# Performance work log

Measured on AMD Instinct MI355X. Metric: run time of the kernel, lower is better.

The kernel has to match this reference:

```python
import jax, jax.numpy as jnp
import numpy as np

D_MODEL = 512
N_HEADS = 16
D_HEAD = D_MODEL // N_HEADS


def _relative_shift(pos_score):
    # pos_score: [B, H, T, T]  (Transformer-XL shift trick)
    B, H, T1, T2 = pos_score.shape
    padded = jnp.pad(pos_score, ((0, 0), (0, 0), (0, 0), (1, 0)))  # [B,H,T1,T2+1]
    padded = padded.reshape(B, H, T2 + 1, T1)
    return padded[:, :, 1:].reshape(B, H, T1, T2)


def setup_inputs() -> dict:
    key = jax.random.key(0)
    ks = jax.random.split(key, 12)
    B, T, D = 4, 1024, D_MODEL
    s = 1.0 / np.sqrt(D)
    return {
        "q": jax.random.normal(ks[0], (B, T, D), jnp.float32),
        "k": jax.random.normal(ks[1], (B, T, D), jnp.float32),
        "v": jax.random.normal(ks[2], (B, T, D), jnp.float32),
        "pos_embedding": jax.random.normal(ks[3], (B, T, D), jnp.float32),
        "Wq": jax.random.normal(ks[4], (D, D), jnp.float32) * s,
        "bq": jnp.zeros((D,), jnp.float32),
        "Wp": jax.random.normal(ks[5], (D, D), jnp.float32) * s,
        "Wf": jax.random.normal(ks[6], (D, D), jnp.float32) * s,
        "bf": jnp.zeros((D,), jnp.float32),
        "u_bias": jax.random.normal(ks[7], (N_HEADS, D_HEAD), jnp.float32) * s,
        "v_bias": jax.random.normal(ks[8], (N_HEADS, D_HEAD), jnp.float32) * s,
    }


def reference(q, k, v, pos_embedding, Wq, bq, Wp, Wf, bf, u_bias, v_bias):
    B, T, D = q.shape
    H, Dh = N_HEADS, D_HEAD
    sqrt_dim = jnp.asarray(np.sqrt(D_MODEL), q.dtype)
    # NOTE: original module uses linear_q for q, k AND v (faithful to source)
    qh = (q @ Wq + bq).reshape(B, T, H, Dh)            # [B,T,H,Dh]
    kh = (k @ Wq + bq).reshape(B, T, H, Dh)
    vh = (v @ Wq + bq).reshape(B, T, H, Dh)
    ph = (pos_embedding @ Wp).reshape(B, T, H, Dh)     # no bias

    content_score = jnp.einsum('bthd,bshd->bhts', qh + u_bias, kh)
    pos_score = jnp.einsum('bthd,bshd->bhts', qh + v_bias, ph)
    pos_score = _relative_shift(pos_score)

    score = (content_score + pos_score) / sqrt_dim     # [B,H,T,T]
    attn = jax.nn.softmax(score, axis=-1)              # dropout identity in eval
    context = jnp.einsum('bhts,bshd->bthd', attn, vh).reshape(B, T, D)
    return context @ Wf + bf
```

## Files before the change

### kernel.cpp

```cpp
#include <hip/hip_runtime.h>
#include <hip/hip_bf16.h>

typedef __bf16 bf16;
typedef bf16 bf16x8 __attribute__((ext_vector_type(8)));
typedef bf16 bf16x4 __attribute__((ext_vector_type(4)));
typedef float f32x4 __attribute__((ext_vector_type(4)));

#define SCALE_INV_SQRT_D 0.04419417382415922f


__global__ __launch_bounds__(256) void prep_kernel(
    const float* __restrict__ Wq, const float* __restrict__ Wp, const float* __restrict__ Wf,
    bf16* __restrict__ WqT, bf16* __restrict__ WpT, bf16* __restrict__ WfT,
    bf16* __restrict__ phx)
{
  const int tid = threadIdx.x;
  if (blockIdx.x < 192) {
    __shared__ bf16 t[64][72];
    const int m = blockIdx.x >> 6;
    const int tb = blockIdx.x & 63;
    const int tr = tb >> 3, tc = tb & 7;
    const float* W = (m == 0) ? Wq : (m == 1) ? Wp : Wf;
    bf16*        O = (m == 0) ? WqT : (m == 1) ? WpT : WfT;
    const int r = tid >> 2, cg = tid & 3;
    {
      const float* src = W + (size_t)(tr * 64 + r) * 512 + tc * 64 + cg * 16;
      f32x4 a = *(const f32x4*)src, b2 = *(const f32x4*)(src + 4);
      f32x4 c = *(const f32x4*)(src + 8), d = *(const f32x4*)(src + 12);
      bf16x8 lo, hi;
#pragma unroll
      for (int j = 0; j < 4; j++) { lo[j] = (bf16)a[j]; lo[4 + j] = (bf16)b2[j]; hi[j] = (bf16)c[j]; hi[4 + j] = (bf16)d[j]; }
      *(bf16x8*)(&t[r][cg * 16])     = lo;
      *(bf16x8*)(&t[r][cg * 16 + 8]) = hi;
    }
    __syncthreads();
    bf16x8 o0, o1;
#pragma unroll
    for (int j = 0; j < 8; j++) { o0[j] = t[cg * 16 + j][r]; o1[j] = t[cg * 16 + 8 + j][r]; }
    bf16* dst = O + (size_t)(tc * 64 + r) * 512 + tr * 64 + cg * 16;
    *(bf16x8*)dst = o0;
    *(bf16x8*)(dst + 8) = o1;
  } else {
    int z = (blockIdx.x - 192) * 256 + tid;
    int bh = z >> 6;
    int rsel = (z >> 5) & 1;
    int d = z & 31;
    phx[((size_t)bh * 2048 + (rsel ? 2047 : 1024)) * 32 + d] = (bf16)0.0f;
  }
}

__global__ __launch_bounds__(256) void proj_gemm(
    const float* __restrict__ q, const float* __restrict__ k, const float* __restrict__ v,
    const float* __restrict__ pos,
    const bf16* __restrict__ WqT, const bf16* __restrict__ WpT, const float* __restrict__ bq,
    bf16* __restrict__ qh, bf16* __restrict__ kh, bf16* __restrict__ vT, bf16* __restrict__ phx)
{
  __shared__ float Asf[128 * 36];
  __shared__ bf16  Bs[128 * 40];
  const int tid = threadIdx.x;
  const int wave = tid >> 6, lane = tid & 63, quad = lane >> 4, ln = lane & 15;
  const int tn = blockIdx.x & 3;
  const int tm = blockIdx.x >> 2;
  const int kind = tm >> 5;
  const int rr0 = (tm & 31) * 128;
  const float* X = (kind == 0) ? q : (kind == 1) ? k : (kind == 2) ? v : pos;
  const bf16* WT = ((kind < 3) ? WqT : WpT) + (size_t)tn * 128 * 512;
  const int qm = (wave & 1) * 64, qn = (wave >> 1) * 64;
  const int srow = tid >> 2, scg = tid & 3;

  f32x4 acc[4][4] = {};

  for (int kk = 0; kk < 16; kk++) {
    const int k0 = kk * 32;
    {
      const float* p0 = X + (size_t)(rr0 + srow) * 512 + k0 + scg * 8;
      const float* p1 = X + (size_t)(rr0 + srow + 64) * 512 + k0 + scg * 8;
      *(f32x4*)(Asf + srow * 36 + scg * 8)            = *(const f32x4*)p0;
      *(f32x4*)(Asf + srow * 36 + scg * 8 + 4)        = *(const f32x4*)(p0 + 4);
      *(f32x4*)(Asf + (srow + 64) * 36 + scg * 8)     = *(const f32x4*)p1;
      *(f32x4*)(Asf + (srow + 64) * 36 + scg * 8 + 4) = *(const f32x4*)(p1 + 4);
    }
    *(bf16x8*)(Bs + srow * 40 + scg * 8)        = *(const bf16x8*)(WT + (size_t)srow * 512 + k0 + scg * 8);
    *(bf16x8*)(Bs + (srow + 64) * 40 + scg * 8) = *(const bf16x8*)(WT + (size_t)(srow + 64) * 512 + k0 + scg * 8);
    __syncthreads();
    bf16x8 af[4], bfm[4];
#pragma unroll
    for (int i = 0; i < 4; i++) {
      f32x4 lo = *(const f32x4*)(Asf + (qm + i * 16 + ln) * 36 + quad * 8);
      f32x4 hi = *(const f32x4*)(Asf + (qm + i * 16 + ln) * 36 + quad * 8 + 4);
      bf16x8 t;
#pragma unroll
      for (int j = 0; j < 4; j++) { t[j] = (bf16)lo[j]; t[4 + j] = (bf16)hi[j]; }
      af[i] = t;
      bfm[i] = *(const bf16x8*)(Bs + (qn + i * 16 + ln) * 40 + quad * 8);
    }
#pragma unroll
    for (int i = 0; i < 4; i++)
#pragma unroll
      for (int j = 0; j < 4; j++)
        acc[i][j] = __builtin_amdgcn_mfma_f32_16x16x32_bf16(af[i], bfm[j], acc[i][j], 0, 0, 0);
    __syncthreads();
  }

#pragma unroll
  for (int i = 0; i < 4; i++)
#pragma unroll
    for (int j = 0; j < 4; j++) {
      const int nn = tn * 128 + qn + j * 16 + ln;
      const int hh = nn >> 5, dd = nn & 31;
      const float bias = (kind < 3) ? bq[nn] : 0.0f;
#pragma unroll
      for (int r = 0; r < 4; r++) {
        const int rr = rr0 + qm + i * 16 + quad * 4 + r;
        const int bb = rr >> 10, tt = rr & 1023;
        const bf16 o = (bf16)(acc[i][j][r] + bias);
        const size_t base = (size_t)(bb * 16 + hh);
        if (kind == 0)      qh[(base * 1024 + tt) * 32 + dd] = o;
        else if (kind == 1) kh[(base * 1024 + tt) * 32 + dd] = o;
        else if (kind == 2) vT[(base * 32 + dd) * 1024 + tt] = o;
        else {
          phx[(base * 2048 + tt) * 32 + dd] = o;
          if (tt <= 1021) phx[(base * 2048 + tt + 1025) * 32 + dd] = o;
        }
      }
    }
}

__global__ __launch_bounds__(256, 4) void attn_kernel(
    const bf16* __restrict__ qh, const bf16* __restrict__ kh,
    const bf16* __restrict__ vT, const bf16* __restrict__ phx,
    const float* __restrict__ u_bias, const float* __restrict__ v_bias,
    bf16* __restrict__ ctx)
{
  __shared__ float fs[4 * 16 * 84];
  __shared__ bf16  pb[4 * 16 * 72];

  const int tid = threadIdx.x;
  const int wave = tid >> 6, lane = tid & 63, quad = lane >> 4, ln = lane & 15;
  const int wg = blockIdx.x;
  const int bh = wg & 63, tq = wg >> 6;
  const int h = bh & 15, b = bh >> 4;
  const int t0 = tq * 64;
  const bf16* qh_h  = qh  + (size_t)bh * 1024 * 32;
  const bf16* kh_h  = kh  + (size_t)bh * 1024 * 32;
  const bf16* vT_h  = vT  + (size_t)bh * 32 * 1024;
  const bf16* phx_h = phx + (size_t)bh * 2048 * 32;

  float* fsw = fs + wave * 16 * 84;
  bf16*  pbw = pb + wave * 16 * 72;

  bf16x8 qu, qva, qvn;
  {
    const int t = t0 + wave * 16 + ln;
    bf16x8 q0 = *(const bf16x8*)(qh_h + (size_t)t * 32 + quad * 8);
    bf16x8 q1 = *(const bf16x8*)(qh_h + (size_t)(t + 1) * 32 + quad * 8);
    const float* ubp = u_bias + h * 32 + quad * 8;
    const float* vbp = v_bias + h * 32 + quad * 8;
#pragma unroll
    for (int j = 0; j < 8; j++) {
      qu[j]  = (bf16)((float)q0[j] + ubp[j]);
      qva[j] = (bf16)((float)q0[j] + vbp[j]);
      qvn[j] = (bf16)((float)q1[j] + vbp[j]);
    }
  }

  f32x4 O0 = {0.f, 0.f, 0.f, 0.f}, O1 = {0.f, 0.f, 0.f, 0.f};
  float m_run = -1e30f, l_run = 0.0f;
  const f32x4 zf = {0.f, 0.f, 0.f, 0.f};

  for (int si = 0; si < 16; si++) {
    const int s0 = si * 64;
    const int j0 = s0 - t0 + 960;
    const int jb0 = j0 + (3 - wave) * 16;

#pragma unroll
    for (int i = 0; i < 5; i++) {
      const int jrow = jb0 + i * 16 + ln;
      bf16x8 pbf = *(const bf16x8*)(phx_h + (size_t)jrow * 32 + quad * 8);
      bf16x8 bsel = (jb0 + i * 16 >= 1024) ? qvn : qva;
      f32x4 f = __builtin_amdgcn_mfma_f32_16x16x32_bf16(pbf, bsel, zf, 0, 0, 0);
      *(f32x4*)(fsw + ln * 84 + i * 16 + quad * 4) = f;
    }

    f32x4 c[4];
#pragma unroll
    for (int cs = 0; cs < 4; cs++) {
      bf16x8 kbf = *(const bf16x8*)(kh_h + (size_t)(s0 + cs * 16 + ln) * 32 + quad * 8);
      c[cs] = __builtin_amdgcn_mfma_f32_16x16x32_bf16(kbf, qu, zf, 0, 0, 0);
    }

    float sc_[4][4];
#pragma unroll
    for (int cs = 0; cs < 4; cs++)
#pragma unroll
      for (int r = 0; r < 4; r++) {
        const int col = cs * 16 + quad * 4 + r - ln + 15;
        sc_[cs][r] = (c[cs][r] + fsw[ln * 84 + col]) * SCALE_INV_SQRT_D;
      }

    float mt = sc_[0][0];
#pragma unroll
    for (int cs = 0; cs < 4; cs++)
#pragma unroll
      for (int r = 0; r < 4; r++) mt = fmaxf(mt, sc_[cs][r]);
    mt = fmaxf(mt, __shfl_xor(mt, 16));
    mt = fmaxf(mt, __shfl_xor(mt, 32));

    const float mnew = fmaxf(m_run, mt);
    const float al = __expf(m_run - mnew);
    float psum = 0.0f;
#pragma unroll
    for (int cs = 0; cs < 4; cs++) {
      bf16x4 pk;
#pragma unroll
      for (int r = 0; r < 4; r++) {
        const float p = __expf(sc_[cs][r] - mnew);
        psum += p;
        pk[r] = (bf16)p;
      }
      *(bf16x4*)(pbw + ln * 72 + cs * 16 + quad * 4) = pk;
    }
    psum += __shfl_xor(psum, 16);
    psum += __shfl_xor(psum, 32);
    l_run = l_run * al + psum;
    m_run = mnew;

#pragma unroll
    for (int r = 0; r < 4; r++) {
      const float alr = __shfl(al, ((lane >> 4) << 2) + r);
      O0[r] *= alr;
      O1[r] *= alr;
    }

#pragma unroll
    for (int kb = 0; kb < 2; kb++) {
      bf16x8 a  = *(const bf16x8*)(pbw + ln * 72 + kb * 32 + quad * 8);
      bf16x8 b0 = *(const bf16x8*)(vT_h + (size_t)ln * 1024 + s0 + kb * 32 + quad * 8);
      bf16x8 b1 = *(const bf16x8*)(vT_h + (size_t)(16 + ln) * 1024 + s0 + kb * 32 + quad * 8);
      O0 = __builtin_amdgcn_mfma_f32_16x16x32_bf16(a, b0, O0, 0, 0, 0);
      O1 = __builtin_amdgcn_mfma_f32_16x16x32_bf16(a, b1, O1, 0, 0, 0);
    }
  }

#pragma unroll
  for (int r = 0; r < 4; r++) {
    const float lr = __shfl(l_run, ((lane >> 4) << 2) + r);
    const float inv = 1.0f / lr;
    const int t = t0 + wave * 16 + quad * 4 + r;
    const size_t o = ((size_t)(b * 1024 + t)) * 512 + h * 32;
    ctx[o + ln]      = (bf16)(O0[r] * inv);
    ctx[o + 16 + ln] = (bf16)(O1[r] * inv);
  }
}

__global__ __launch_bounds__(256) void out_gemm(
    const bf16* __restrict__ ctx, const bf16* __restrict__ WfT, const float* __restrict__ bfv,
    float* __restrict__ out)
{
  __shared__ bf16 As[64 * 40];
  __shared__ bf16 Bs[128 * 40];
  const int tid = threadIdx.x;
  const int wave = tid >> 6, lane = tid & 63, quad = lane >> 4, ln = lane & 15;
  const int tn = blockIdx.x & 3;
  const int tm = blockIdx.x >> 2;
  const int rr0 = tm * 64;
  const bf16* WT = WfT + (size_t)tn * 128 * 512;
  const int qm = (wave & 1) * 32, qn = (wave >> 1) * 64;
  const int srow = tid >> 2, scg = tid & 3;

  f32x4 acc[2][4] = {};
  for (int kk = 0; kk < 16; kk++) {
    const int k0 = kk * 32;
    *(bf16x8*)(As + srow * 40 + scg * 8)        = *(const bf16x8*)(ctx + (size_t)(rr0 + srow) * 512 + k0 + scg * 8);
    *(bf16x8*)(Bs + srow * 40 + scg * 8)        = *(const bf16x8*)(WT + (size_t)srow * 512 + k0 + scg * 8);
    *(bf16x8*)(Bs + (srow + 64) * 40 + scg * 8) = *(const bf16x8*)(WT + (size_t)(srow + 64) * 512 + k0 + scg * 8);
    __syncthreads();
    bf16x8 af[2], bfm[4];
#pragma unroll
    for (int i = 0; i < 2; i++)
      af[i] = *(const bf16x8*)(As + (qm + i * 16 + ln) * 40 + quad * 8);
#pragma unroll
    for (int j = 0; j < 4; j++)
      bfm[j] = *(const bf16x8*)(Bs + (qn + j * 16 + ln) * 40 + quad * 8);
#pragma unroll
    for (int i = 0; i < 2; i++)
#pragma unroll
      for (int j = 0; j < 4; j++)
        acc[i][j] = __builtin_amdgcn_mfma_f32_16x16x32_bf16(af[i], bfm[j], acc[i][j], 0, 0, 0);
    __syncthreads();
  }

#pragma unroll
  for (int i = 0; i < 2; i++)
#pragma unroll
    for (int j = 0; j < 4; j++) {
      const int nn = tn * 128 + qn + j * 16 + ln;
      const float bias = bfv[nn];
#pragma unroll
      for (int r = 0; r < 4; r++) {
        const int rr = rr0 + qm + i * 16 + quad * 4 + r;
        out[(size_t)rr * 512 + nn] = acc[i][j][r] + bias;
      }
    }
}

extern "C" void kernel_launch(void* const* d_in, const int* in_sizes, int n_in,
                              void* d_out, int out_size, void* d_ws, size_t ws_size,
                              hipStream_t stream) {
  const float* q   = (const float*)d_in[0];
  const float* k   = (const float*)d_in[1];
  const float* v   = (const float*)d_in[2];
  const float* pe  = (const float*)d_in[3];
  const float* Wq  = (const float*)d_in[4];
  const float* bq  = (const float*)d_in[5];
  const float* Wp  = (const float*)d_in[6];
  const float* Wf  = (const float*)d_in[7];
  const float* bfv = (const float*)d_in[8];
  const float* ub  = (const float*)d_in[9];
  const float* vb  = (const float*)d_in[10];

  bf16* ws  = (bf16*)d_ws;
  bf16* qh  = ws;
  bf16* kh  = qh + 2097152;
  bf16* vT  = kh + 2097152;
  bf16* phx = vT + 2097152;
  bf16* ctx = phx + 4194304;
  bf16* WqT = ctx + 2097152;
  bf16* WpT = WqT + 262144;
  bf16* WfT = WpT + 262144;

  prep_kernel<<<208, 256, 0, stream>>>(Wq, Wp, Wf, WqT, WpT, WfT, phx);
  proj_gemm<<<512, 256, 0, stream>>>(q, k, v, pe, WqT, WpT, bq, qh, kh, vT, phx);
  attn_kernel<<<1024, 256, 0, stream>>>(qh, kh, vT, phx, ub, vb, ctx);
  out_gemm<<<256, 256, 0, stream>>>(ctx, WfT, bfv, (float*)d_out);
}
```

Baseline: 195.2 us.

## Fold softmax scale into query, use exp2, vectorize projection epilogue stores

The 1/sqrt(d)·log2(e) factor is folded into the biased query vectors, so the per-score multiply disappears and the softmax uses exp2f instead of __expf. The projection GEMM swaps the MFMA operand roles so each lane holds four consecutive output features, which lets the epilogue write bf16x4 vector stores and load bias as a float4 instead of scalar stores. The P staging buffer row stride is padded from 72 to 88 to change the LDS bank pattern. Rounding the scaled query to bf16 shifts numerics slightly, and the transposed vT stores stay scalar.

```diff
diff --git a/kernel.cpp b/kernel.cpp
--- a/kernel.cpp
+++ b/kernel.cpp
@@ -6,7 +6,7 @@
 typedef bf16 bf16x4 __attribute__((ext_vector_type(4)));
 typedef float f32x4 __attribute__((ext_vector_type(4)));
 
-#define SCALE_INV_SQRT_D 0.04419417382415922f
+#define SCALE_LOG2 0.06376237f
 
 
 __global__ __launch_bounds__(256) void prep_kernel(
@@ -65,7 +65,8 @@
   const int rr0 = (tm & 31) * 128;
   const float* X = (kind == 0) ? q : (kind == 1) ? k : (kind == 2) ? v : pos;
   const bf16* WT = ((kind < 3) ? WqT : WpT) + (size_t)tn * 128 * 512;
-  const int qm = (wave & 1) * 64, qn = (wave >> 1) * 64;
+  const int qn_ = (wave & 1) * 64;
+  const int qr_ = (wave >> 1) * 64;
   const int srow = tid >> 2, scg = tid & 3;
 
   f32x4 acc[4][4] = {};
@@ -83,47 +84,50 @@
     *(bf16x8*)(Bs + srow * 40 + scg * 8)        = *(const bf16x8*)(WT + (size_t)srow * 512 + k0 + scg * 8);
     *(bf16x8*)(Bs + (srow + 64) * 40 + scg * 8) = *(const bf16x8*)(WT + (size_t)(srow + 64) * 512 + k0 + scg * 8);
     __syncthreads();
-    bf16x8 af[4], bfm[4];
+    bf16x8 wf[4], xf[4];
 #pragma unroll
     for (int i = 0; i < 4; i++) {
-      f32x4 lo = *(const f32x4*)(Asf + (qm + i * 16 + ln) * 36 + quad * 8);
-      f32x4 hi = *(const f32x4*)(Asf + (qm + i * 16 + ln) * 36 + quad * 8 + 4);
+      wf[i] = *(const bf16x8*)(Bs + (qn_ + i * 16 + ln) * 40 + quad * 8);
+      f32x4 lo = *(const f32x4*)(Asf + (qr_ + i * 16 + ln) * 36 + quad * 8);
+      f32x4 hi = *(const f32x4*)(Asf + (qr_ + i * 16 + ln) * 36 + quad * 8 + 4);
       bf16x8 t;
 #pragma unroll
       for (int j = 0; j < 4; j++) { t[j] = (bf16)lo[j]; t[4 + j] = (bf16)hi[j]; }
-      af[i] = t;
-      bfm[i] = *(const bf16x8*)(Bs + (qn + i * 16 + ln) * 40 + quad * 8);
+      xf[i] = t;
     }
 #pragma unroll
     for (int i = 0; i < 4; i++)
 #pragma unroll
       for (int j = 0; j < 4; j++)
-        acc[i][j] = __builtin_amdgcn_mfma_f32_16x16x32_bf16(af[i], bfm[j], acc[i][j], 0, 0, 0);
-    __syncthreads();
-  }
-
-#pragma unroll
-  for (int i = 0; i < 4; i++)
+        acc[i][j] = __builtin_amdgcn_mfma_f32_16x16x32_bf16(wf[i], xf[j], acc[i][j], 0, 0, 0);
+    __syncthreads();
+  }
+
+#pragma unroll
+  for (int i = 0; i < 4; i++) {
+    const int nn0 = tn * 128 + qn_ + i * 16 + quad * 4;
+    const int dd0 = nn0 & 31, hh = nn0 >> 5;
+    f32x4 b4 = {0.f, 0.f, 0.f, 0.f};
+    if (kind < 3) b4 = *(const f32x4*)(bq + nn0);
 #pragma unroll
     for (int j = 0; j < 4; j++) {
-      const int nn = tn * 128 + qn + j * 16 + ln;
-      const int hh = nn >> 5, dd = nn & 31;
-      const float bias = (kind < 3) ? bq[nn] : 0.0f;
-#pragma unroll
-      for (int r = 0; r < 4; r++) {
-        const int rr = rr0 + qm + i * 16 + quad * 4 + r;
-        const int bb = rr >> 10, tt = rr & 1023;
-        const bf16 o = (bf16)(acc[i][j][r] + bias);
-        const size_t base = (size_t)(bb * 16 + hh);
-        if (kind == 0)      qh[(base * 1024 + tt) * 32 + dd] = o;
-        else if (kind == 1) kh[(base * 1024 + tt) * 32 + dd] = o;
-        else if (kind == 2) vT[(base * 32 + dd) * 1024 + tt] = o;
-        else {
-          phx[(base * 2048 + tt) * 32 + dd] = o;
-          if (tt <= 1021) phx[(base * 2048 + tt + 1025) * 32 + dd] = o;
-        }
+      const int rr = rr0 + qr_ + j * 16 + ln;
+      const int bb = rr >> 10, tt = rr & 1023;
+      const size_t base = (size_t)(bb * 16 + hh);
+      bf16x4 pk;
+#pragma unroll
+      for (int r = 0; r < 4; r++) pk[r] = (bf16)(acc[i][j][r] + b4[r]);
+      if (kind == 0)      *(bf16x4*)(qh + (base * 1024 + tt) * 32 + dd0) = pk;
+      else if (kind == 1) *(bf16x4*)(kh + (base * 1024 + tt) * 32 + dd0) = pk;
+      else if (kind == 2) {
+#pragma unroll
+        for (int r = 0; r < 4; r++) vT[(base * 32 + dd0 + r) * 1024 + tt] = pk[r];
+      } else {
+        *(bf16x4*)(phx + (base * 2048 + tt) * 32 + dd0) = pk;
+        if (tt <= 1021) *(bf16x4*)(phx + (base * 2048 + tt + 1025) * 32 + dd0) = pk;
       }
     }
+  }
 }
 
 __global__ __launch_bounds__(256, 4) void attn_kernel(
@@ -133,7 +137,7 @@
     bf16* __restrict__ ctx)
 {
   __shared__ float fs[4 * 16 * 84];
-  __shared__ bf16  pb[4 * 16 * 72];
+  __shared__ bf16  pb[4 * 16 * 88];
 
   const int tid = threadIdx.x;
   const int wave = tid >> 6, lane = tid & 63, quad = lane >> 4, ln = lane & 15;
@@ -147,7 +151,7 @@
   const bf16* phx_h = phx + (size_t)bh * 2048 * 32;
 
   float* fsw = fs + wave * 16 * 84;
-  bf16*  pbw = pb + wave * 16 * 72;
+  bf16*  pbw = pb + wave * 16 * 88;
 
   bf16x8 qu, qva, qvn;
   {
@@ -158,9 +162,9 @@
     const float* vbp = v_bias + h * 32 + quad * 8;
 #pragma unroll
     for (int j = 0; j < 8; j++) {
-      qu[j]  = (bf16)((float)q0[j] + ubp[j]);
-      qva[j] = (bf16)((float)q0[j] + vbp[j]);
-      qvn[j] = (bf16)((float)q1[j] + vbp[j]);
+      qu[j]  = (bf16)(((float)q0[j] + ubp[j]) * SCALE_LOG2);
+      qva[j] = (bf16)(((float)q0[j] + vbp[j]) * SCALE_LOG2);
+      qvn[j] = (bf16)(((float)q1[j] + vbp[j]) * SCALE_LOG2);
     }
   }
 
@@ -195,7 +199,7 @@
 #pragma unroll
       for (int r = 0; r < 4; r++) {
         const int col = cs * 16 + quad * 4 + r - ln + 15;
-        sc_[cs][r] = (c[cs][r] + fsw[ln * 84 + col]) * SCALE_INV_SQRT_D;
+        sc_[cs][r] = c[cs][r] + fsw[ln * 84 + col];
       }
 
     float mt = sc_[0][0];
@@ -207,18 +211,18 @@
     mt = fmaxf(mt, __shfl_xor(mt, 32));
 
     const float mnew = fmaxf(m_run, mt);
-    const float al = __expf(m_run - mnew);
+    const float al = exp2f(m_run - mnew);
     float psum = 0.0f;
 #pragma unroll
     for (int cs = 0; cs < 4; cs++) {
       bf16x4 pk;
 #pragma unroll
       for (int r = 0; r < 4; r++) {
-        const float p = __expf(sc_[cs][r] - mnew);
+        const float p = exp2f(sc_[cs][r] - mnew);
         psum += p;
         pk[r] = (bf16)p;
       }
-      *(bf16x4*)(pbw + ln * 72 + cs * 16 + quad * 4) = pk;
+      *(bf16x4*)(pbw + ln * 88 + cs * 16 + quad * 4) = pk;
     }
     psum += __shfl_xor(psum, 16);
     psum += __shfl_xor(psum, 32);
@@ -234,7 +238,7 @@
 
 #pragma unroll
     for (int kb = 0; kb < 2; kb++) {
-      bf16x8 a  = *(const bf16x8*)(pbw + ln * 72 + kb * 32 + quad * 8);
+      bf16x8 a  = *(const bf16x8*)(pbw + ln * 88 + kb * 32 + quad * 8);
       bf16x8 b0 = *(const bf16x8*)(vT_h + (size_t)ln * 1024 + s0 + kb * 32 + quad * 8);
       bf16x8 b1 = *(const bf16x8*)(vT_h + (size_t)(16 + ln) * 1024 + s0 + kb * 32 + quad * 8);
       O0 = __builtin_amdgcn_mfma_f32_16x16x32_bf16(a, b0, O0, 0, 0, 0);
```

Measured after the change: 192.7 us. About the same (-1.3%).
